# Kernel optimization log

Measured on AMD Instinct MI355X. Metric: run time of the kernel, lower is better.

The kernel has to match this reference:

```python
import jax, jax.numpy as jnp
import numpy as np

OUT_DIM = 64
NUM_HEADS = 8
HID = NUM_HEADS * OUT_DIM  # 512
ALPHA = 0.01  # leaky relu slope
N_NODES = 20000
N_EDGES = 100000
MP_LEN = 3


def setup_inputs() -> dict:
    key = jax.random.key(0)
    ks = jax.random.split(key, 8)
    s = 1.0 / np.sqrt(HID)
    return {
        "features": jax.random.normal(ks[0], (N_NODES, OUT_DIM), jnp.float32),
        "W_ih": jax.random.normal(ks[1], (3 * HID, OUT_DIM), jnp.float32) * s,
        "W_hh": jax.random.normal(ks[2], (3 * HID, HID), jnp.float32) * s,
        "b_ih": jax.random.normal(ks[3], (3 * HID,), jnp.float32) * s,
        "b_hh": jax.random.normal(ks[4], (3 * HID,), jnp.float32) * s,
        "attn": jax.random.normal(ks[5], (NUM_HEADS, OUT_DIM), jnp.float32) * 0.1,
        "edge_metapath_indices": jax.random.randint(ks[6], (N_EDGES, MP_LEN), 0, N_NODES),
        "edge_dst": jax.random.randint(ks[7], (N_EDGES,), 0, N_NODES),
    }


def _gru_last_hidden(x_seq, W_ih, W_hh, b_ih, b_hh):
    """x_seq: [L, E, D] -> final hidden [E, HID] (torch nn.GRU math, h0=0)."""
    E = x_seq.shape[1]
    h0 = jnp.zeros((E, HID), x_seq.dtype)

    def step(h, x):
        gi = x @ W_ih.T + b_ih  # [E, 3*HID]
        gh = h @ W_hh.T + b_hh  # [E, 3*HID]
        i_r, i_z, i_n = jnp.split(gi, 3, axis=-1)
        h_r, h_z, h_n = jnp.split(gh, 3, axis=-1)
        r = jax.nn.sigmoid(i_r + h_r)
        z = jax.nn.sigmoid(i_z + h_z)
        n = jnp.tanh(i_n + r * h_n)
        h_new = (1.0 - z) * n + z * h
        return h_new, None

    h_last, _ = jax.lax.scan(step, h0, x_seq)
    return h_last


def reference(features, W_ih, W_hh, b_ih, b_hh, attn,
              edge_metapath_indices, edge_dst):
    N = features.shape[0]
    # gather metapath node features: [E, L, D] -> GRU over L
    edata = features[edge_metapath_indices]
    h = _gru_last_hidden(jnp.transpose(edata, (1, 0, 2)), W_ih, W_hh, b_ih, b_hh)
    eft = h.reshape(-1, NUM_HEADS, OUT_DIM)  # [E, H, D]
    # attention logits per edge/head + leaky relu
    a = jnp.sum(eft * attn[None], axis=-1)  # [E, H]
    a = jnp.where(a >= 0, a, ALPHA * a)
    # edge softmax grouped by destination node
    amax = jax.ops.segment_max(a, edge_dst, num_segments=N)  # [N, H]
    ea = jnp.exp(a - amax[edge_dst])
    denom = jax.ops.segment_sum(ea, edge_dst, num_segments=N)  # [N, H]
    alpha = ea / denom[edge_dst]  # [E, H]
    # weighted message aggregation (sum) to destination nodes
    msg = eft * alpha[:, :, None]  # [E, H, D]
    ret = jax.ops.segment_sum(msg, edge_dst, num_segments=N)  # [N, H, D]
    return ret
```

## Files before the change

kernel.cpp:

```cpp
#include <hip/hip_runtime.h>
#include <hip/hip_bf16.h>

#define N_NODES 20000
#define N_EDGES 100000
#define HID 512
#define G3 1536
#define NH 8
#define OD 64

typedef __hip_bfloat16 bf16;
typedef __attribute__((ext_vector_type(8))) short bf16x8;
typedef __attribute__((ext_vector_type(4))) float f32x4;

__device__ __forceinline__ float frcp(float x) { return __builtin_amdgcn_rcpf(x); }
__device__ __forceinline__ float fsig(float x) { return frcp(1.0f + __expf(-x)); }
__device__ __forceinline__ float ftanh(float x) { return 1.0f - 2.0f * frcp(__expf(2.0f * x) + 1.0f); }
__device__ __forceinline__ float b2f(bf16 b) { return __bfloat162float(b); }
__device__ __forceinline__ bf16 f2b(float f) { return __float2bfloat16(f); }
__device__ __forceinline__ float bs2f(short s) {
    return __uint_as_float(((unsigned)(unsigned short)s) << 16);
}
__device__ __forceinline__ float us2f(unsigned short s) {
    return __uint_as_float(((unsigned)s) << 16);
}
__device__ __forceinline__ short f2bs(float f) {
    bf16 b = __float2bfloat16(f);
    return *reinterpret_cast<short*>(&b);
}
__device__ __forceinline__ unsigned ford(float f) {
    unsigned u = __float_as_uint(f);
    return (u & 0x80000000u) ? ~u : (u | 0x80000000u);
}
__device__ __forceinline__ float iford(unsigned u) {
    return __uint_as_float((u & 0x80000000u) ? (u & 0x7fffffffu) : ~u);
}

__device__ __forceinline__ void g2l16(const void* g, void* l) {
#if __has_builtin(__builtin_amdgcn_global_load_lds)
    __builtin_amdgcn_global_load_lds((const __attribute__((address_space(1))) char*)g,
                                     (__attribute__((address_space(3))) char*)l, 16, 0, 0);
#else
    *(bf16x8*)l = *(const bf16x8*)g;
#endif
}


__global__ __launch_bounds__(256) void k_prep(const float* __restrict__ Whh,
                                              const float* __restrict__ Wih,
                                              bf16* __restrict__ WTs,
                                              float* __restrict__ WIT) {
    int t = blockIdx.x * 256 + threadIdx.x;
    if (t < 98304) {
        int T = t >> 10, c = (t >> 6) & 15, l = t & 63;
        int n = T * 16 + (l & 15);
        int k = c * 32 + ((l >> 4) << 3);
        const float* src = Whh + (size_t)n * 512 + k;
        bf16x8 v;
#pragma unroll
        for (int j = 0; j < 8; ++j) v[j] = f2bs(src[j]);
        *(bf16x8*)(WTs + (size_t)t * 8) = v;
    } else {
        int u = t - 98304;
        int d = u / 1536, j = u % 1536;
        WIT[u] = Wih[(size_t)j * 64 + d];
    }
}

__global__ __launch_bounds__(256) void k_count(const int* __restrict__ dst,
                                               unsigned* __restrict__ cnt) {
    int e = blockIdx.x * 256 + threadIdx.x;
    if (e < N_EDGES) atomicAdd(&cnt[dst[e]], 1u);
}

#define SCAN_CH 79
__global__ __launch_bounds__(256) void k_scan(const unsigned* __restrict__ cnt,
                                              unsigned* __restrict__ base,
                                              unsigned* __restrict__ cursor) {
    __shared__ unsigned ls[256];
    int t = threadIdx.x;
    int s0 = t * SCAN_CH;
    int s1 = s0 + SCAN_CH < N_NODES ? s0 + SCAN_CH : N_NODES;
    unsigned s = 0;
    for (int i = s0; i < s1; ++i) s += cnt[i];
    ls[t] = s;
    __syncthreads();
    for (int d = 1; d < 256; d <<= 1) {
        unsigned v = (t >= d) ? ls[t - d] : 0u;
        __syncthreads();
        ls[t] += v;
        __syncthreads();
    }
    unsigned run = ls[t] - s;
    for (int i = s0; i < s1; ++i) {
        base[i] = run; cursor[i] = run; run += cnt[i];
    }
    if (t == 255) base[N_NODES] = ls[255];
}

__global__ __launch_bounds__(256) void k_fill(const int* __restrict__ dst,
                                              unsigned* __restrict__ cursor,
                                              unsigned* __restrict__ csr) {
    int e = blockIdx.x * 256 + threadIdx.x;
    if (e < N_EDGES) {
        unsigned p = atomicAdd(&cursor[dst[e]], 1u);
        csr[p] = (unsigned)e;
    }
}

__global__ __launch_bounds__(256) void k_gi(const float* __restrict__ feat,
                                            const float* __restrict__ WIT,
                                            const float* __restrict__ b_ih,
                                            const float* __restrict__ b_hh,
                                            bf16* __restrict__ G,
                                            bf16* __restrict__ H1) {
    __shared__ float fs[16][64];
    const int n0 = blockIdx.x * 16;
    const int k = blockIdx.y * 256 + threadIdx.x;
    for (int i = threadIdx.x; i < 16 * 64; i += 256)
        fs[0][i] = feat[(size_t)n0 * 64 + i];
    __syncthreads();
    float acc[3][16];
#pragma unroll
    for (int g = 0; g < 3; ++g) {
        float b = b_ih[g * 512 + k];
#pragma unroll
        for (int e = 0; e < 16; ++e) acc[g][e] = b;
    }
    for (int d = 0; d < 64; d += 4) {
        float w[3][4];
#pragma unroll
        for (int u = 0; u < 4; ++u)
#pragma unroll
            for (int g = 0; g < 3; ++g)
                w[g][u] = WIT[(size_t)(d + u) * G3 + g * 512 + k];
#pragma unroll
        for (int e = 0; e < 16; ++e) {
            float4 f = *(const float4*)&fs[e][d];
#pragma unroll
            for (int g = 0; g < 3; ++g)
                acc[g][e] += w[g][0] * f.x + w[g][1] * f.y + w[g][2] * f.z + w[g][3] * f.w;
        }
    }
    const float br = b_hh[k], bz = b_hh[512 + k], bn = b_hh[1024 + k];
#pragma unroll
    for (int e = 0; e < 16; ++e) {
        bf16* dst = G + (size_t)(n0 + e) * G3 + k * 3;
        dst[0] = f2b(acc[0][e]);
        dst[1] = f2b(acc[1][e]);
        dst[2] = f2b(acc[2][e]);
        float r1 = fsig(acc[0][e] + br);
        float z1 = fsig(acc[1][e] + bz);
        float n1 = ftanh(acc[2][e] + r1 * bn);
        H1[(size_t)(n0 + e) * HID + k] = f2b((1.0f - z1) * n1);
    }
}

__global__ __launch_bounds__(256, 4) void k_gh2(const bf16* __restrict__ H1,
                                                const bf16* __restrict__ WTs,
                                                const float* __restrict__ b_hh,
                                                bf16* __restrict__ GH2) {
    __shared__ short Bs[2][8192];
    const int tid = threadIdx.x;
    const int wave = tid >> 6, lane = tid & 63;
    const int m0 = blockIdx.x * 64;
    const int k0 = (lane >> 4) << 3;

    bf16x8 afrag[16];
    {
        int row = m0 + wave * 16 + (lane & 15);
        int ar = row < N_NODES ? row : N_NODES - 1;
#pragma unroll
        for (int c = 0; c < 16; ++c)
            afrag[c] = *(const bf16x8*)(H1 + (size_t)ar * HID + c * 32 + k0);
    }

    const int col = lane & 15;
    const int qb = (lane >> 4) << 2;
    const int boff = lane * 8;

#pragma unroll
    for (int i = 0; i < 4; ++i) {
        int q = tid + i * 256;
        g2l16(WTs + (size_t)q * 8, &Bs[0][q * 8]);
    }
    __syncthreads();

    int cur = 0;
    for (int jt = 0; jt < 32; ++jt) {
        const int cj = jt * 16 + col;
        f32x4 a0 = {0, 0, 0, 0}, a1 = {0, 0, 0, 0}, a2 = {0, 0, 0, 0};
        const float br = b_hh[cj], bz = b_hh[512 + cj], bn = b_hh[1024 + cj];
        {
#pragma unroll
            for (int i = 0; i < 4; ++i) {
                int q = tid + i * 256;
                g2l16(WTs + 262144 + (size_t)jt * 8192 + q * 8, &Bs[cur ^ 1][q * 8]);
            }
            const short* cb = &Bs[cur][0];
#pragma unroll
            for (int c = 0; c < 16; ++c) {
                bf16x8 b = *(const bf16x8*)&cb[c * 512 + boff];
                a0 = __builtin_amdgcn_mfma_f32_16x16x32_bf16(afrag[c], b, a0, 0, 0, 0);
            }
            __syncthreads();
            cur ^= 1;
        }
        {
#pragma unroll
            for (int i = 0; i < 4; ++i) {
                int q = tid + i * 256;
                g2l16(WTs + 524288 + (size_t)jt * 8192 + q * 8, &Bs[cur ^ 1][q * 8]);
            }
            const short* cb = &Bs[cur][0];
#pragma unroll
            for (int c = 0; c < 16; ++c) {
                bf16x8 b = *(const bf16x8*)&cb[c * 512 + boff];
                a1 = __builtin_amdgcn_mfma_f32_16x16x32_bf16(afrag[c], b, a1, 0, 0, 0);
            }
            __syncthreads();
            cur ^= 1;
        }
        {
            if (jt < 31) {
#pragma unroll
                for (int i = 0; i < 4; ++i) {
                    int q = tid + i * 256;
                    g2l16(WTs + (size_t)(jt + 1) * 8192 + q * 8, &Bs[cur ^ 1][q * 8]);
                }
            }
            const short* cb = &Bs[cur][0];
#pragma unroll
            for (int c = 0; c < 16; ++c) {
                bf16x8 b = *(const bf16x8*)&cb[c * 512 + boff];
                a2 = __builtin_amdgcn_mfma_f32_16x16x32_bf16(afrag[c], b, a2, 0, 0, 0);
            }
#pragma unroll
            for (int q = 0; q < 4; ++q) {
                int e = m0 + wave * 16 + qb + q;
                if (e < N_NODES) {
                    bf16* dst = GH2 + (size_t)e * G3 + cj * 3;
                    dst[0] = f2b(a0[q] + br);
                    dst[1] = f2b(a1[q] + bz);
                    dst[2] = f2b(a2[q] + bn);
                }
            }
            __syncthreads();
            cur ^= 1;
        }
    }
}

__global__ __launch_bounds__(256) void k_h2(const bf16* __restrict__ G,
                                            const bf16* __restrict__ GH2,
                                            const bf16* __restrict__ H1,
                                            const int* __restrict__ emi,
                                            bf16* __restrict__ h2) {
    size_t i = (size_t)blockIdx.x * 256 + threadIdx.x;
    int e = (int)(i >> 6);
    int kc = (int)(i & 63) * 8;
    int i0 = emi[(size_t)e * 3 + 0];
    int i1 = emi[(size_t)e * 3 + 1];
    const bf16* g1p = G + (size_t)i1 * G3 + kc * 3;
    const bf16* ghp = GH2 + (size_t)i0 * G3 + kc * 3;
    bf16x8 h1v = *(const bf16x8*)(H1 + (size_t)i0 * HID + kc);
    short s1[24], sh[24];
    {
        bf16x8 a0 = *(const bf16x8*)g1p, a1 = *(const bf16x8*)(g1p + 8), a2 = *(const bf16x8*)(g1p + 16);
        bf16x8 c0 = *(const bf16x8*)ghp, c1 = *(const bf16x8*)(ghp + 8), c2 = *(const bf16x8*)(ghp + 16);
#pragma unroll
        for (int j = 0; j < 8; ++j) {
            s1[j] = a0[j]; s1[8 + j] = a1[j]; s1[16 + j] = a2[j];
            sh[j] = c0[j]; sh[8 + j] = c1[j]; sh[16 + j] = c2[j];
        }
    }
    bf16x8 out;
#pragma unroll
    for (int j = 0; j < 8; ++j) {
        float r = fsig(bs2f(s1[j * 3 + 0]) + bs2f(sh[j * 3 + 0]));
        float z = fsig(bs2f(s1[j * 3 + 1]) + bs2f(sh[j * 3 + 1]));
        float n = ftanh(bs2f(s1[j * 3 + 2]) + r * bs2f(sh[j * 3 + 2]));
        out[j] = f2bs((1.0f - z) * n + z * bs2f(h1v[j]));
    }
    *(bf16x8*)(h2 + (size_t)e * HID + kc) = out;
}

__global__ __launch_bounds__(256, 4) void k_gemm3(const bf16* __restrict__ G,
                                                  const bf16* __restrict__ WTs,
                                                  const float* __restrict__ b_hh,
                                                  const int* __restrict__ emi,
                                                  bf16* __restrict__ h2) {
    __shared__ short Bs[2][8192];
    __shared__ int si2[64];
    const int tid = threadIdx.x;
    const int wave = tid >> 6, lane = tid & 63;
    const int m0 = blockIdx.x * 64;
    if (tid < 64) {
        int e = m0 + tid;
        si2[tid] = emi[(size_t)(e < N_EDGES ? e : N_EDGES - 1) * 3 + 2];
    }
    const int k0 = (lane >> 4) << 3;

    bf16x8 afrag[16];
    {
        int row = m0 + wave * 16 + (lane & 15);
        int ar = row < N_EDGES ? row : N_EDGES - 1;
#pragma unroll
        for (int c = 0; c < 16; ++c)
            afrag[c] = *(const bf16x8*)(h2 + (size_t)ar * HID + c * 32 + k0);
    }

    const int col = lane & 15;
    const int qb = (lane >> 4) << 2;
    const int boff = lane * 8;

#pragma unroll
    for (int i = 0; i < 4; ++i) {
        int q = tid + i * 256;
        g2l16(WTs + (size_t)q * 8, &Bs[0][q * 8]);
    }
    __syncthreads();

    int cur = 0;
    for (int jt = 0; jt < 32; ++jt) {
        const int cj = jt * 16 + col;
        f32x4 a0 = {0, 0, 0, 0}, a1 = {0, 0, 0, 0}, a2 = {0, 0, 0, 0};
        float br, bz, bn;
        unsigned short pg[4][3], ph[4];
        {
            br = b_hh[cj]; bz = b_hh[512 + cj]; bn = b_hh[1024 + cj];
#pragma unroll
            for (int q = 0; q < 4; ++q) {
                int li = wave * 16 + qb + q;
                int e = m0 + li;
                int ec = e < N_EDGES ? e : N_EDGES - 1;
                const unsigned short* g2p =
                    (const unsigned short*)(G + (size_t)si2[li] * G3 + cj * 3);
                pg[q][0] = g2p[0]; pg[q][1] = g2p[1]; pg[q][2] = g2p[2];
                ph[q] = ((const unsigned short*)h2)[(size_t)ec * HID + cj];
            }
#pragma unroll
            for (int i = 0; i < 4; ++i) {
                int q = tid + i * 256;
                g2l16(WTs + 262144 + (size_t)jt * 8192 + q * 8, &Bs[cur ^ 1][q * 8]);
            }
            const short* cb = &Bs[cur][0];
#pragma unroll
            for (int c = 0; c < 16; ++c) {
                bf16x8 b = *(const bf16x8*)&cb[c * 512 + boff];
                a0 = __builtin_amdgcn_mfma_f32_16x16x32_bf16(afrag[c], b, a0, 0, 0, 0);
            }
            __syncthreads();
            cur ^= 1;
        }
        {
#pragma unroll
            for (int i = 0; i < 4; ++i) {
                int q = tid + i * 256;
                g2l16(WTs + 524288 + (size_t)jt * 8192 + q * 8, &Bs[cur ^ 1][q * 8]);
            }
            const short* cb = &Bs[cur][0];
#pragma unroll
            for (int c = 0; c < 16; ++c) {
                bf16x8 b = *(const bf16x8*)&cb[c * 512 + boff];
                a1 = __builtin_amdgcn_mfma_f32_16x16x32_bf16(afrag[c], b, a1, 0, 0, 0);
            }
            __syncthreads();
            cur ^= 1;
        }
        {
            if (jt < 31) {
#pragma unroll
                for (int i = 0; i < 4; ++i) {
                    int q = tid + i * 256;
                    g2l16(WTs + (size_t)(jt + 1) * 8192 + q * 8, &Bs[cur ^ 1][q * 8]);
                }
            }
            const short* cb = &Bs[cur][0];
#pragma unroll
            for (int c = 0; c < 16; ++c) {
                bf16x8 b = *(const bf16x8*)&cb[c * 512 + boff];
                a2 = __builtin_amdgcn_mfma_f32_16x16x32_bf16(afrag[c], b, a2, 0, 0, 0);
            }
#pragma unroll
            for (int q = 0; q < 4; ++q) {
                int e = m0 + wave * 16 + qb + q;
                if (e < N_EDGES) {
                    float r = fsig(us2f(pg[q][0]) + a0[q] + br);
                    float z = fsig(us2f(pg[q][1]) + a1[q] + bz);
                    float ng = ftanh(us2f(pg[q][2]) + r * (a2[q] + bn));
                    h2[(size_t)e * HID + cj] = f2b((1.0f - z) * ng + z * us2f(ph[q]));
                }
            }
            __syncthreads();
            cur ^= 1;
        }
    }
}

__global__ __launch_bounds__(256) void k_logits(const bf16* __restrict__ eft,
                                                const float* __restrict__ attn,
                                                const int* __restrict__ dst,
                                                float* __restrict__ a,
                                                unsigned* __restrict__ amax) {
    int i = blockIdx.x * 256 + threadIdx.x;
    int e = i >> 3, h = i & 7;
    const __hip_bfloat162* f2 = (const __hip_bfloat162*)(eft + (size_t)e * HID + h * OD);
    const float* at = attn + h * OD;
    float s = 0.f;
#pragma unroll
    for (int d = 0; d < OD / 2; ++d) {
        float2 fv = __bfloat1622float2(f2[d]);
        s += fv.x * at[2 * d] + fv.y * at[2 * d + 1];
    }
    s = (s >= 0.f) ? s : 0.01f * s;
    a[i] = s;
    atomicMax(&amax[(size_t)dst[e] * NH + h], ford(s));
}

__global__ __launch_bounds__(256) void k_ea(const int* __restrict__ dst,
                                            const unsigned* __restrict__ amax,
                                            float* __restrict__ a,
                                            float* __restrict__ denom) {
    int i = blockIdx.x * 256 + threadIdx.x;
    int e = i >> 3, h = i & 7;
    float m = iford(amax[(size_t)dst[e] * NH + h]);
    float v = __expf(a[i] - m);
    a[i] = v;
    atomicAdd(&denom[(size_t)dst[e] * NH + h], v);
}

__global__ __launch_bounds__(256) void k_out(const bf16* __restrict__ eft,
                                             const float* __restrict__ a,
                                             const float* __restrict__ denom,
                                             const unsigned* __restrict__ base,
                                             const unsigned* __restrict__ csr,
                                             float* __restrict__ out) {
    int n = blockIdx.x;
    int k = blockIdx.y * 256 + threadIdx.x;
    int h = k >> 6;
    unsigned b0 = base[n], b1 = base[n + 1];
    float rden = (b1 > b0) ? frcp(denom[(size_t)n * NH + h]) : 0.0f;
    float acc = 0.f;
    for (unsigned i = b0; i < b1; ++i) {
        unsigned e = csr[i];
        float al = a[(size_t)e * NH + h];
        acc += b2f(eft[(size_t)e * HID + k]) * al;
    }
    out[(size_t)n * HID + k] = acc * rden;
}

extern "C" void kernel_launch(void* const* d_in, const int* in_sizes, int n_in,
                              void* d_out, int out_size, void* d_ws, size_t ws_size,
                              hipStream_t stream) {
    (void)in_sizes; (void)n_in; (void)ws_size; (void)out_size;
    const float* feat = (const float*)d_in[0];
    const float* W_ih = (const float*)d_in[1];
    const float* W_hh = (const float*)d_in[2];
    const float* b_ih = (const float*)d_in[3];
    const float* b_hh = (const float*)d_in[4];
    const float* attn = (const float*)d_in[5];
    const int* emi = (const int*)d_in[6];
    const int* dst = (const int*)d_in[7];
    float* out = (float*)d_out;

    char* ws = (char*)d_ws;
    bf16* G = (bf16*)ws;
    bf16* GH2 = (bf16*)(ws + 61440000);
    bf16* h2 = (bf16*)(ws + 122880000);
    bf16* WTs = (bf16*)(ws + 225280000);
    float* WIT = (float*)(ws + 226852864);
    float* a = (float*)(ws + 227246080);
    unsigned* amax = (unsigned*)(ws + 230446080);
    float* denom = (float*)(ws + 231086080);
    unsigned* cnt = (unsigned*)(ws + 231726080);
    unsigned* base = (unsigned*)(ws + 231806080);
    unsigned* cursor = (unsigned*)(ws + 231886088);
    unsigned* csr = (unsigned*)(ws + 231966088);
    bf16* H1 = (bf16*)(ws + 232366088);

    (void)hipMemsetAsync(amax, 0, 1360000, stream);

    k_prep<<<768, 256, 0, stream>>>(W_hh, W_ih, WTs, WIT);
    k_count<<<391, 256, 0, stream>>>(dst, cnt);
    k_scan<<<1, 256, 0, stream>>>(cnt, base, cursor);
    k_fill<<<391, 256, 0, stream>>>(dst, cursor, csr);
    k_gi<<<dim3(1250, 2), 256, 0, stream>>>(feat, WIT, b_ih, b_hh, G, H1);
    k_gh2<<<313, 256, 0, stream>>>(H1, WTs, b_hh, GH2);
    k_h2<<<25000, 256, 0, stream>>>(G, GH2, H1, emi, h2);
    k_gemm3<<<1563, 256, 0, stream>>>(G, WTs, b_hh, emi, h2);
    k_logits<<<3125, 256, 0, stream>>>(h2, attn, dst, a, amax);
    k_ea<<<3125, 256, 0, stream>>>(dst, amax, a, denom);
    k_out<<<dim3(N_NODES, 2), 256, 0, stream>>>(h2, a, denom, base, csr, out);
}
```

Baseline: 764.9 us.

## Switch final GRU gemm to 32x32 MFMA with 128-row edge tiles

Rewrites the third-step recurrent GEMM to use 32x32x16 bf16 MFMA instructions. Each block now covers 128 edges instead of 64, with a new pre-swizzled weight layout (WT32) generated in the prep kernel. The larger tile halves how often each block reloads the weight tiles into LDS and uses fewer, larger MFMA instructions. The cost is higher register pressure (occupancy bound lowered to 2 waves per SIMD) and gather loads for the gate epilogue that are no longer issued ahead of the MFMA loop.

Measured after the change: 872.3 us. +14.0%, slower.

```diff
diff --git a/kernel.cpp b/kernel.cpp
--- a/kernel.cpp
+++ b/kernel.cpp
@@ -11,6 +11,7 @@
 typedef __hip_bfloat16 bf16;
 typedef __attribute__((ext_vector_type(8))) short bf16x8;
 typedef __attribute__((ext_vector_type(4))) float f32x4;
+typedef __attribute__((ext_vector_type(16))) float f32x16;
 
 __device__ __forceinline__ float frcp(float x) { return __builtin_amdgcn_rcpf(x); }
 __device__ __forceinline__ float fsig(float x) { return frcp(1.0f + __expf(-x)); }
@@ -48,6 +49,7 @@
 __global__ __launch_bounds__(256) void k_prep(const float* __restrict__ Whh,
                                               const float* __restrict__ Wih,
                                               bf16* __restrict__ WTs,
+                                              bf16* __restrict__ WT32,
                                               float* __restrict__ WIT) {
     int t = blockIdx.x * 256 + threadIdx.x;
     if (t < 98304) {
@@ -59,8 +61,19 @@
 #pragma unroll
         for (int j = 0; j < 8; ++j) v[j] = f2bs(src[j]);
         *(bf16x8*)(WTs + (size_t)t * 8) = v;
+    } else if (t < 196608) {
+        int u = t - 98304;
+        int l = u & 63, c = (u >> 6) & 31, jg = u >> 11;
+        int jt = jg & 15, g = jg >> 4;
+        int n = g * 512 + jt * 32 + (l & 31);
+        int k = c * 16 + ((l >> 5) << 3);
+        const float* src = Whh + (size_t)n * 512 + k;
+        bf16x8 v;
+#pragma unroll
+        for (int j = 0; j < 8; ++j) v[j] = f2bs(src[j]);
+        *(bf16x8*)(WT32 + (size_t)u * 8) = v;
     } else {
-        int u = t - 98304;
+        int u = t - 196608;
         int d = u / 1536, j = u % 1536;
         WIT[u] = Wih[(size_t)j * 64 + d];
     }
@@ -284,112 +297,108 @@
     *(bf16x8*)(h2 + (size_t)e * HID + kc) = out;
 }
 
-__global__ __launch_bounds__(256, 4) void k_gemm3(const bf16* __restrict__ G,
-                                                  const bf16* __restrict__ WTs,
+__global__ __launch_bounds__(256, 2) void k_gemm3(const bf16* __restrict__ G,
+                                                  const bf16* __restrict__ WT32,
                                                   const float* __restrict__ b_hh,
                                                   const int* __restrict__ emi,
                                                   bf16* __restrict__ h2) {
-    __shared__ short Bs[2][8192];
-    __shared__ int si2[64];
+    __shared__ short Bs[2][16384];
+    __shared__ int si2[128];
     const int tid = threadIdx.x;
     const int wave = tid >> 6, lane = tid & 63;
-    const int m0 = blockIdx.x * 64;
-    if (tid < 64) {
+    const int m0 = blockIdx.x * 128;
+    if (tid < 128) {
         int e = m0 + tid;
         si2[tid] = emi[(size_t)(e < N_EDGES ? e : N_EDGES - 1) * 3 + 2];
     }
-    const int k0 = (lane >> 4) << 3;
-
-    bf16x8 afrag[16];
+    const int ka = (lane >> 5) << 3;
+
+    bf16x8 afrag[32];
     {
-        int row = m0 + wave * 16 + (lane & 15);
+        int row = m0 + wave * 32 + (lane & 31);
         int ar = row < N_EDGES ? row : N_EDGES - 1;
 #pragma unroll
-        for (int c = 0; c < 16; ++c)
-            afrag[c] = *(const bf16x8*)(h2 + (size_t)ar * HID + c * 32 + k0);
-    }
-
-    const int col = lane & 15;
-    const int qb = (lane >> 4) << 2;
+        for (int c = 0; c < 32; ++c)
+            afrag[c] = *(const bf16x8*)(h2 + (size_t)ar * HID + c * 16 + ka);
+    }
+
+    const int col = lane & 31;
+    const int hi = lane >> 5;
     const int boff = lane * 8;
 
 #pragma unroll
-    for (int i = 0; i < 4; ++i) {
+    for (int i = 0; i < 8; ++i) {
         int q = tid + i * 256;
-        g2l16(WTs + (size_t)q * 8, &Bs[0][q * 8]);
+        g2l16(WT32 + (size_t)q * 8, &Bs[0][q * 8]);
     }
     __syncthreads();
 
     int cur = 0;
-    for (int jt = 0; jt < 32; ++jt) {
-        const int cj = jt * 16 + col;
-        f32x4 a0 = {0, 0, 0, 0}, a1 = {0, 0, 0, 0}, a2 = {0, 0, 0, 0};
-        float br, bz, bn;
-        unsigned short pg[4][3], ph[4];
+    for (int jt = 0; jt < 16; ++jt) {
+        const int cj = jt * 32 + col;
+        f32x16 a0, a1, a2;
+#pragma unroll
+        for (int q = 0; q < 16; ++q) { a0[q] = 0.f; a1[q] = 0.f; a2[q] = 0.f; }
         {
-            br = b_hh[cj]; bz = b_hh[512 + cj]; bn = b_hh[1024 + cj];
-#pragma unroll
-            for (int q = 0; q < 4; ++q) {
-                int li = wave * 16 + qb + q;
+#pragma unroll
+            for (int i = 0; i < 8; ++i) {
+                int q = tid + i * 256;
+                g2l16(WT32 + 262144 + (size_t)jt * 16384 + q * 8, &Bs[cur ^ 1][q * 8]);
+            }
+            const short* cb = &Bs[cur][0];
+#pragma unroll
+            for (int c = 0; c < 32; ++c) {
+                bf16x8 b = *(const bf16x8*)&cb[c * 512 + boff];
+                a0 = __builtin_amdgcn_mfma_f32_32x32x16_bf16(afrag[c], b, a0, 0, 0, 0);
+            }
+            __syncthreads();
+            cur ^= 1;
+        }
+        {
+#pragma unroll
+            for (int i = 0; i < 8; ++i) {
+                int q = tid + i * 256;
+                g2l16(WT32 + 524288 + (size_t)jt * 16384 + q * 8, &Bs[cur ^ 1][q * 8]);
+            }
+            const short* cb = &Bs[cur][0];
+#pragma unroll
+            for (int c = 0; c < 32; ++c) {
+                bf16x8 b = *(const bf16x8*)&cb[c * 512 + boff];
+                a1 = __builtin_amdgcn_mfma_f32_32x32x16_bf16(afrag[c], b, a1, 0, 0, 0);
+            }
+            __syncthreads();
+            cur ^= 1;
+        }
+        {
+            if (jt < 15) {
+#pragma unroll
+                for (int i = 0; i < 8; ++i) {
+                    int q = tid + i * 256;
+                    g2l16(WT32 + (size_t)(jt + 1) * 16384 + q * 8, &Bs[cur ^ 1][q * 8]);
+                }
+            }
+            const short* cb = &Bs[cur][0];
+#pragma unroll
+            for (int c = 0; c < 32; ++c) {
+                bf16x8 b = *(const bf16x8*)&cb[c * 512 + boff];
+                a2 = __builtin_amdgcn_mfma_f32_32x32x16_bf16(afrag[c], b, a2, 0, 0, 0);
+            }
+            const float br = b_hh[cj], bz = b_hh[512 + cj], bn = b_hh[1024 + cj];
+#pragma unroll
+            for (int reg = 0; reg < 16; ++reg) {
+                int r = (reg & 3) + 8 * (reg >> 2) + 4 * hi;
+                int li = wave * 32 + r;
                 int e = m0 + li;
                 int ec = e < N_EDGES ? e : N_EDGES - 1;
-                const unsigned short* g2p =
+                const unsigned short* gp =
                     (const unsigned short*)(G + (size_t)si2[li] * G3 + cj * 3);
-                pg[q][0] = g2p[0]; pg[q][1] = g2p[1]; pg[q][2] = g2p[2];
-                ph[q] = ((const unsigned short*)h2)[(size_t)ec * HID + cj];
-            }
-#pragma unroll
-            for (int i = 0; i < 4; ++i) {
-                int q = tid + i * 256;
-                g2l16(WTs + 262144 + (size_t)jt * 8192 + q * 8, &Bs[cur ^ 1][q * 8]);
-            }
-            const short* cb = &Bs[cur][0];
-#pragma unroll
-            for (int c = 0; c < 16; ++c) {
-                bf16x8 b = *(const bf16x8*)&cb[c * 512 + boff];
-                a0 = __builtin_amdgcn_mfma_f32_16x16x32_bf16(afrag[c], b, a0, 0, 0, 0);
-            }
-            __syncthreads();
-            cur ^= 1;
-        }
-        {
-#pragma unroll
-            for (int i = 0; i < 4; ++i) {
-                int q = tid + i * 256;
-                g2l16(WTs + 524288 + (size_t)jt * 8192 + q * 8, &Bs[cur ^ 1][q * 8]);
-            }
-            const short* cb = &Bs[cur][0];
-#pragma unroll
-            for (int c = 0; c < 16; ++c) {
-                bf16x8 b = *(const bf16x8*)&cb[c * 512 + boff];
-                a1 = __builtin_amdgcn_mfma_f32_16x16x32_bf16(afrag[c], b, a1, 0, 0, 0);
-            }
-            __syncthreads();
-            cur ^= 1;
-        }
-        {
-            if (jt < 31) {
-#pragma unroll
-                for (int i = 0; i < 4; ++i) {
-                    int q = tid + i * 256;
-                    g2l16(WTs + (size_t)(jt + 1) * 8192 + q * 8, &Bs[cur ^ 1][q * 8]);
-                }
-            }
-            const short* cb = &Bs[cur][0];
-#pragma unroll
-            for (int c = 0; c < 16; ++c) {
-                bf16x8 b = *(const bf16x8*)&cb[c * 512 + boff];
-                a2 = __builtin_amdgcn_mfma_f32_16x16x32_bf16(afrag[c], b, a2, 0, 0, 0);
-            }
-#pragma unroll
-            for (int q = 0; q < 4; ++q) {
-                int e = m0 + wave * 16 + qb + q;
-                if (e < N_EDGES) {
-                    float r = fsig(us2f(pg[q][0]) + a0[q] + br);
-                    float z = fsig(us2f(pg[q][1]) + a1[q] + bz);
-                    float ng = ftanh(us2f(pg[q][2]) + r * (a2[q] + bn));
-                    h2[(size_t)e * HID + cj] = f2b((1.0f - z) * ng + z * us2f(ph[q]));
-                }
+                unsigned short g0 = gp[0], g1 = gp[1], g2v = gp[2];
+                unsigned short hv = ((const unsigned short*)h2)[(size_t)ec * HID + cj];
+                float rr = fsig(us2f(g0) + a0[reg] + br);
+                float zz = fsig(us2f(g1) + a1[reg] + bz);
+                float nn = ftanh(us2f(g2v) + rr * (a2[reg] + bn));
+                if (e < N_EDGES)
+                    h2[(size_t)e * HID + cj] = f2b((1.0f - zz) * nn + zz * us2f(hv));
             }
             __syncthreads();
             cur ^= 1;
@@ -477,17 +486,18 @@
     unsigned* cursor = (unsigned*)(ws + 231886088);
     unsigned* csr = (unsigned*)(ws + 231966088);
     bf16* H1 = (bf16*)(ws + 232366088);
+    bf16* WT32 = (bf16*)(ws + 227246080);
 
     (void)hipMemsetAsync(amax, 0, 1360000, stream);
 
-    k_prep<<<768, 256, 0, stream>>>(W_hh, W_ih, WTs, WIT);
+    k_prep<<<1152, 256, 0, stream>>>(W_hh, W_ih, WTs, WT32, WIT);
     k_count<<<391, 256, 0, stream>>>(dst, cnt);
     k_scan<<<1, 256, 0, stream>>>(cnt, base, cursor);
     k_fill<<<391, 256, 0, stream>>>(dst, cursor, csr);
     k_gi<<<dim3(1250, 2), 256, 0, stream>>>(feat, WIT, b_ih, b_hh, G, H1);
     k_gh2<<<313, 256, 0, stream>>>(H1, WTs, b_hh, GH2);
     k_h2<<<25000, 256, 0, stream>>>(G, GH2, H1, emi, h2);
-    k_gemm3<<<1563, 256, 0, stream>>>(G, WTs, b_hh, emi, h2);
+    k_gemm3<<<782, 256, 0, stream>>>(G, WT32, b_hh, emi, h2);
     k_logits<<<3125, 256, 0, stream>>>(h2, attn, dst, a, amax);
     k_ea<<<3125, 256, 0, stream>>>(dst, amax, a, denom);
     k_out<<<dim3(N_NODES, 2), 256, 0, stream>>>(h2, a, denom, base, csr, out);
```

## Double per-wave M tile in GRU GEMM kernels to reuse shared B tiles

Applied to the files above, without the earlier changes.

Each wave in k_gh2 and k_gemm3 now holds two 16-row A fragments and issues two MFMAs per loaded B fragment, doubling block M to 128 rows and halving grid size. This amortises the LDS weight-tile streaming and barriers over twice as many rows. In exchange register pressure doubles (launch bounds drop to 2 blocks/CU), and k_gh2 launches only 157 blocks, which may underfill the GPU.

After: 801.4 us. 4.8% more time.

```diff
diff --git a/kernel.cpp b/kernel.cpp
--- a/kernel.cpp
+++ b/kernel.cpp
@@ -155,23 +155,24 @@
     }
 }
 
-__global__ __launch_bounds__(256, 4) void k_gh2(const bf16* __restrict__ H1,
+__global__ __launch_bounds__(256, 2) void k_gh2(const bf16* __restrict__ H1,
                                                 const bf16* __restrict__ WTs,
                                                 const float* __restrict__ b_hh,
                                                 bf16* __restrict__ GH2) {
     __shared__ short Bs[2][8192];
     const int tid = threadIdx.x;
     const int wave = tid >> 6, lane = tid & 63;
-    const int m0 = blockIdx.x * 64;
+    const int m0 = blockIdx.x * 128;
     const int k0 = (lane >> 4) << 3;
 
-    bf16x8 afrag[16];
-    {
-        int row = m0 + wave * 16 + (lane & 15);
+    bf16x8 afrag[2][16];
+#pragma unroll
+    for (int t = 0; t < 2; ++t) {
+        int row = m0 + wave * 32 + t * 16 + (lane & 15);
         int ar = row < N_NODES ? row : N_NODES - 1;
 #pragma unroll
         for (int c = 0; c < 16; ++c)
-            afrag[c] = *(const bf16x8*)(H1 + (size_t)ar * HID + c * 32 + k0);
+            afrag[t][c] = *(const bf16x8*)(H1 + (size_t)ar * HID + c * 32 + k0);
     }
 
     const int col = lane & 15;
@@ -188,7 +189,11 @@
     int cur = 0;
     for (int jt = 0; jt < 32; ++jt) {
         const int cj = jt * 16 + col;
-        f32x4 a0 = {0, 0, 0, 0}, a1 = {0, 0, 0, 0}, a2 = {0, 0, 0, 0};
+        f32x4 acc[2][3];
+#pragma unroll
+        for (int t = 0; t < 2; ++t)
+#pragma unroll
+            for (int g = 0; g < 3; ++g) acc[t][g] = (f32x4){0, 0, 0, 0};
         const float br = b_hh[cj], bz = b_hh[512 + cj], bn = b_hh[1024 + cj];
         {
 #pragma unroll
@@ -200,7 +205,8 @@
 #pragma unroll
             for (int c = 0; c < 16; ++c) {
                 bf16x8 b = *(const bf16x8*)&cb[c * 512 + boff];
-                a0 = __builtin_amdgcn_mfma_f32_16x16x32_bf16(afrag[c], b, a0, 0, 0, 0);
+                acc[0][0] = __builtin_amdgcn_mfma_f32_16x16x32_bf16(afrag[0][c], b, acc[0][0], 0, 0, 0);
+                acc[1][0] = __builtin_amdgcn_mfma_f32_16x16x32_bf16(afrag[1][c], b, acc[1][0], 0, 0, 0);
             }
             __syncthreads();
             cur ^= 1;
@@ -215,7 +221,8 @@
 #pragma unroll
             for (int c = 0; c < 16; ++c) {
                 bf16x8 b = *(const bf16x8*)&cb[c * 512 + boff];
-                a1 = __builtin_amdgcn_mfma_f32_16x16x32_bf16(afrag[c], b, a1, 0, 0, 0);
+                acc[0][1] = __builtin_amdgcn_mfma_f32_16x16x32_bf16(afrag[0][c], b, acc[0][1], 0, 0, 0);
+                acc[1][1] = __builtin_amdgcn_mfma_f32_16x16x32_bf16(afrag[1][c], b, acc[1][1], 0, 0, 0);
             }
             __syncthreads();
             cur ^= 1;
@@ -232,18 +239,21 @@
 #pragma unroll
             for (int c = 0; c < 16; ++c) {
                 bf16x8 b = *(const bf16x8*)&cb[c * 512 + boff];
-                a2 = __builtin_amdgcn_mfma_f32_16x16x32_bf16(afrag[c], b, a2, 0, 0, 0);
-            }
-#pragma unroll
-            for (int q = 0; q < 4; ++q) {
-                int e = m0 + wave * 16 + qb + q;
-                if (e < N_NODES) {
-                    bf16* dst = GH2 + (size_t)e * G3 + cj * 3;
-                    dst[0] = f2b(a0[q] + br);
-                    dst[1] = f2b(a1[q] + bz);
-                    dst[2] = f2b(a2[q] + bn);
+                acc[0][2] = __builtin_amdgcn_mfma_f32_16x16x32_bf16(afrag[0][c], b, acc[0][2], 0, 0, 0);
+                acc[1][2] = __builtin_amdgcn_mfma_f32_16x16x32_bf16(afrag[1][c], b, acc[1][2], 0, 0, 0);
+            }
+#pragma unroll
+            for (int t = 0; t < 2; ++t)
+#pragma unroll
+                for (int q = 0; q < 4; ++q) {
+                    int e = m0 + wave * 32 + t * 16 + qb + q;
+                    if (e < N_NODES) {
+                        bf16* dst = GH2 + (size_t)e * G3 + cj * 3;
+                        dst[0] = f2b(acc[t][0][q] + br);
+                        dst[1] = f2b(acc[t][1][q] + bz);
+                        dst[2] = f2b(acc[t][2][q] + bn);
+                    }
                 }
-            }
             __syncthreads();
             cur ^= 1;
         }
@@ -284,29 +294,30 @@
     *(bf16x8*)(h2 + (size_t)e * HID + kc) = out;
 }
 
-__global__ __launch_bounds__(256, 4) void k_gemm3(const bf16* __restrict__ G,
+__global__ __launch_bounds__(256, 2) void k_gemm3(const bf16* __restrict__ G,
                                                   const bf16* __restrict__ WTs,
                                                   const float* __restrict__ b_hh,
                                                   const int* __restrict__ emi,
                                                   bf16* __restrict__ h2) {
     __shared__ short Bs[2][8192];
-    __shared__ int si2[64];
+    __shared__ int si2[128];
     const int tid = threadIdx.x;
     const int wave = tid >> 6, lane = tid & 63;
-    const int m0 = blockIdx.x * 64;
-    if (tid < 64) {
+    const int m0 = blockIdx.x * 128;
+    if (tid < 128) {
         int e = m0 + tid;
         si2[tid] = emi[(size_t)(e < N_EDGES ? e : N_EDGES - 1) * 3 + 2];
     }
     const int k0 = (lane >> 4) << 3;
 
-    bf16x8 afrag[16];
-    {
-        int row = m0 + wave * 16 + (lane & 15);
+    bf16x8 afrag[2][16];
+#pragma unroll
+    for (int t = 0; t < 2; ++t) {
+        int row = m0 + wave * 32 + t * 16 + (lane & 15);
         int ar = row < N_EDGES ? row : N_EDGES - 1;
 #pragma unroll
         for (int c = 0; c < 16; ++c)
-            afrag[c] = *(const bf16x8*)(h2 + (size_t)ar * HID + c * 32 + k0);
+            afrag[t][c] = *(const bf16x8*)(h2 + (size_t)ar * HID + c * 32 + k0);
     }
 
     const int col = lane & 15;
@@ -323,21 +334,27 @@
     int cur = 0;
     for (int jt = 0; jt < 32; ++jt) {
         const int cj = jt * 16 + col;
-        f32x4 a0 = {0, 0, 0, 0}, a1 = {0, 0, 0, 0}, a2 = {0, 0, 0, 0};
+        f32x4 acc[2][3];
+#pragma unroll
+        for (int t = 0; t < 2; ++t)
+#pragma unroll
+            for (int g = 0; g < 3; ++g) acc[t][g] = (f32x4){0, 0, 0, 0};
         float br, bz, bn;
-        unsigned short pg[4][3], ph[4];
+        unsigned short pg[2][4][3], ph[2][4];
         {
             br = b_hh[cj]; bz = b_hh[512 + cj]; bn = b_hh[1024 + cj];
 #pragma unroll
-            for (int q = 0; q < 4; ++q) {
-                int li = wave * 16 + qb + q;
-                int e = m0 + li;
-                int ec = e < N_EDGES ? e : N_EDGES - 1;
-                const unsigned short* g2p =
-                    (const unsigned short*)(G + (size_t)si2[li] * G3 + cj * 3);
-                pg[q][0] = g2p[0]; pg[q][1] = g2p[1]; pg[q][2] = g2p[2];
-                ph[q] = ((const unsigned short*)h2)[(size_t)ec * HID + cj];
-            }
+            for (int t = 0; t < 2; ++t)
+#pragma unroll
+                for (int q = 0; q < 4; ++q) {
+                    int li = wave * 32 + t * 16 + qb + q;
+                    int e = m0 + li;
+                    int ec = e < N_EDGES ? e : N_EDGES - 1;
+                    const unsigned short* g2p =
+                        (const unsigned short*)(G + (size_t)si2[li] * G3 + cj * 3);
+                    pg[t][q][0] = g2p[0]; pg[t][q][1] = g2p[1]; pg[t][q][2] = g2p[2];
+                    ph[t][q] = ((const unsigned short*)h2)[(size_t)ec * HID + cj];
+                }
 #pragma unroll
             for (int i = 0; i < 4; ++i) {
                 int q = tid + i * 256;
@@ -347,7 +364,8 @@
 #pragma unroll
             for (int c = 0; c < 16; ++c) {
                 bf16x8 b = *(const bf16x8*)&cb[c * 512 + boff];
-                a0 = __builtin_amdgcn_mfma_f32_16x16x32_bf16(afrag[c], b, a0, 0, 0, 0);
+                acc[0][0] = __builtin_amdgcn_mfma_f32_16x16x32_bf16(afrag[0][c], b, acc[0][0], 0, 0, 0);
+                acc[1][0] = __builtin_amdgcn_mfma_f32_16x16x32_bf16(afrag[1][c], b, acc[1][0], 0, 0, 0);
             }
             __syncthreads();
             cur ^= 1;
@@ -362,7 +380,8 @@
 #pragma unroll
             for (int c = 0; c < 16; ++c) {
                 bf16x8 b = *(const bf16x8*)&cb[c * 512 + boff];
-                a1 = __builtin_amdgcn_mfma_f32_16x16x32_bf16(afrag[c], b, a1, 0, 0, 0);
+                acc[0][1] = __builtin_amdgcn_mfma_f32_16x16x32_bf16(afrag[0][c], b, acc[0][1], 0, 0, 0);
+                acc[1][1] = __builtin_amdgcn_mfma_f32_16x16x32_bf16(afrag[1][c], b, acc[1][1], 0, 0, 0);
             }
             __syncthreads();
             cur ^= 1;
@@ -379,18 +398,21 @@
 #pragma unroll
             for (int c = 0; c < 16; ++c) {
                 bf16x8 b = *(const bf16x8*)&cb[c * 512 + boff];
-                a2 = __builtin_amdgcn_mfma_f32_16x16x32_bf16(afrag[c], b, a2, 0, 0, 0);
-            }
-#pragma unroll
-            for (int q = 0; q < 4; ++q) {
-                int e = m0 + wave * 16 + qb + q;
-                if (e < N_EDGES) {
-                    float r = fsig(us2f(pg[q][0]) + a0[q] + br);
-                    float z = fsig(us2f(pg[q][1]) + a1[q] + bz);
-                    float ng = ftanh(us2f(pg[q][2]) + r * (a2[q] + bn));
-                    h2[(size_t)e * HID + cj] = f2b((1.0f - z) * ng + z * us2f(ph[q]));
+                acc[0][2] = __builtin_amdgcn_mfma_f32_16x16x32_bf16(afrag[0][c], b, acc[0][2], 0, 0, 0);
+                acc[1][2] = __builtin_amdgcn_mfma_f32_16x16x32_bf16(afrag[1][c], b, acc[1][2], 0, 0, 0);
+            }
+#pragma unroll
+            for (int t = 0; t < 2; ++t)
+#pragma unroll
+                for (int q = 0; q < 4; ++q) {
+                    int e = m0 + wave * 32 + t * 16 + qb + q;
+                    if (e < N_EDGES) {
+                        float r = fsig(us2f(pg[t][q][0]) + acc[t][0][q] + br);
+                        float z = fsig(us2f(pg[t][q][1]) + acc[t][1][q] + bz);
+                        float ng = ftanh(us2f(pg[t][q][2]) + r * (acc[t][2][q] + bn));
+                        h2[(size_t)e * HID + cj] = f2b((1.0f - z) * ng + z * us2f(ph[t][q]));
+                    }
                 }
-            }
             __syncthreads();
             cur ^= 1;
         }
@@ -485,9 +507,9 @@
     k_scan<<<1, 256, 0, stream>>>(cnt, base, cursor);
     k_fill<<<391, 256, 0, stream>>>(dst, cursor, csr);
     k_gi<<<dim3(1250, 2), 256, 0, stream>>>(feat, WIT, b_ih, b_hh, G, H1);
-    k_gh2<<<313, 256, 0, stream>>>(H1, WTs, b_hh, GH2);
+    k_gh2<<<157, 256, 0, stream>>>(H1, WTs, b_hh, GH2);
     k_h2<<<25000, 256, 0, stream>>>(G, GH2, H1, emi, h2);
-    k_gemm3<<<1563, 256, 0, stream>>>(G, WTs, b_hh, emi, h2);
+    k_gemm3<<<782, 256, 0, stream>>>(G, WTs, b_hh, emi, h2);
     k_logits<<<3125, 256, 0, stream>>>(h2, attn, dst, a, amax);
     k_ea<<<3125, 256, 0, stream>>>(dst, amax, a, denom);
     k_out<<<dim3(N_NODES, 2), 256, 0, stream>>>(h2, a, denom, base, csr, out);
```
